# Performance work log

Measured on AMD Instinct MI355X. Metric: run time of the kernel, lower is better.

## Reference

```python
import jax, jax.numpy as jnp
import numpy as np
from jax import lax

K = 5
SCALE = 100.0
IN_CHN = 128
OUT_CHN = 128
KS = 3
STRIDE = 1
PAD = 1
N_W = OUT_CHN * IN_CHN * KS * KS


def setup_inputs() -> dict:
    key = jax.random.key(0)
    k1, k2, k3, k4, k5 = jax.random.split(key, 5)
    x = jax.random.normal(k1, (32, IN_CHN, 56, 56), dtype=jnp.float32)
    Alpha = jax.random.uniform(k2, (OUT_CHN, 1, 1), dtype=jnp.float32)
    # xavier-normal-ish init for M, Z
    M = jax.random.normal(k3, (OUT_CHN, IN_CHN, KS, KS), dtype=jnp.float32) * 0.05
    Z = jax.random.normal(k4, (K, OUT_CHN, IN_CHN, KS, KS), dtype=jnp.float32) * 0.05
    # rv ~ N(0, 1/sqrt(scale)) of shape (1, K); sample is all-zeros so the random branch is taken
    rv = jax.random.normal(k5, (1, K), dtype=jnp.float32) / np.float32(np.sqrt(SCALE))
    return {"x": x, "Alpha": Alpha, "M": M, "Z": Z, "rv": rv}


def reference(x, Alpha, M, Z, rv):
    # --- SDP weight synthesis (normalization is done under no_grad in torch) ---
    m = M.reshape(N_W)                # (N,)
    z = Z.reshape(K, N_W)             # (K, N)
    A = m * m + jnp.sum(z * z, axis=0) / SCALE
    inv = lax.rsqrt(A)
    m_n = m * inv
    z_n = z * inv
    w = (rv @ z_n + m_n).reshape(OUT_CHN, IN_CHN, KS, KS)  # (O,I,k,k)
    # --- sign binarization of weights and activations (ReCU) ---
    bw = jnp.sign(w)
    ba = jnp.sign(x)
    # --- conv2d, NCHW/OIHW ---
    out = lax.conv_general_dilated(
        ba, bw,
        window_strides=(STRIDE, STRIDE),
        padding=[(PAD, PAD), (PAD, PAD)],
        dimension_numbers=("NCHW", "OIHW", "NCHW"),
    )
    out = out * Alpha  # Alpha (O,1,1) broadcasts over (B,O,H,W)
    return out
```

## Files before the change

kernel.cpp:

```cpp
#include <hip/hip_runtime.h>
#include <stdint.h>

typedef unsigned int u32;
typedef unsigned long long u64;

#define NW      147456
#define HW      3136
#define PADW    58
#define PADHW   3364

#define NBI     365
#define NOG     8
#define NBB     440

__global__ __launch_bounds__(256) void k_wsynth(
    const float* __restrict__ M, const float* __restrict__ Z,
    const float* __restrict__ rv, u32* __restrict__ wb)
{
  __shared__ float sw[1152];
  int o = blockIdx.x;
  int t = threadIdx.x;
  float r0 = rv[0], r1 = rv[1], r2 = rv[2], r3 = rv[3], r4 = rv[4];
  const float4* M4 = (const float4*)M;
  const float4* Z4 = (const float4*)Z;
  float4* sw4 = (float4*)sw;

  for (int j = t; j < 288; j += 256) {
    float4 a = M4[o * 288 + j];
    float4 z;
    z = Z4[0 * 36864 + o * 288 + j];
    a.x = fmaf(r0, z.x, a.x); a.y = fmaf(r0, z.y, a.y);
    a.z = fmaf(r0, z.z, a.z); a.w = fmaf(r0, z.w, a.w);
    z = Z4[1 * 36864 + o * 288 + j];
    a.x = fmaf(r1, z.x, a.x); a.y = fmaf(r1, z.y, a.y);
    a.z = fmaf(r1, z.z, a.z); a.w = fmaf(r1, z.w, a.w);
    z = Z4[2 * 36864 + o * 288 + j];
    a.x = fmaf(r2, z.x, a.x); a.y = fmaf(r2, z.y, a.y);
    a.z = fmaf(r2, z.z, a.z); a.w = fmaf(r2, z.w, a.w);
    z = Z4[3 * 36864 + o * 288 + j];
    a.x = fmaf(r3, z.x, a.x); a.y = fmaf(r3, z.y, a.y);
    a.z = fmaf(r3, z.z, a.z); a.w = fmaf(r3, z.w, a.w);
    z = Z4[4 * 36864 + o * 288 + j];
    a.x = fmaf(r4, z.x, a.x); a.y = fmaf(r4, z.y, a.y);
    a.z = fmaf(r4, z.z, a.z); a.w = fmaf(r4, z.w, a.w);
    sw4[j] = a;
  }
  __syncthreads();

  if (t < 36) {
    int tap = t >> 2;
    int wd  = t & 3;
    u32 bits = 0;
#pragma unroll
    for (int c = 0; c < 32; ++c) {
      float v = sw[(wd * 32 + c) * 9 + tap];
      bits |= (v > 0.0f ? 1u : 0u) << c;
    }
    wb[(o * 9 + tap) * 4 + wd] = bits;
  }
}

__global__ __launch_bounds__(256) void k_apack(
    const float* __restrict__ x, u32* __restrict__ abw)
{
  int t     = threadIdx.x;
  int chunk = blockIdx.x % 53;
  int b     = blockIdx.x / 53;
  int px    = chunk * 64 + (t & 63);
  int g     = t >> 6;
  if (px >= PADHW) return;
  int ph = px / PADW;
  int pw = px - ph * PADW;
  u32 bits = 0;
  if (ph >= 1 && ph <= 56 && pw >= 1 && pw <= 56) {
    const float* xp = x + (size_t)b * (128 * HW) + (size_t)g * (32 * HW)
                        + (ph - 1) * 56 + (pw - 1);
#pragma unroll
    for (int c = 0; c < 32; ++c)
      bits |= (xp[(size_t)c * HW] > 0.0f ? 1u : 0u) << c;
  }
  abw[((size_t)b * PADHW + px) * 4 + g] = bits;
}

__global__ __launch_bounds__(256) void k_conv(
    const uint4* __restrict__ ab, const uint4* __restrict__ wbg,
    const float* __restrict__ Alpha, float* __restrict__ out)
{
  int bx  = blockIdx.x;
  int tid = threadIdx.x;

  if (bx < NBI * NOG) {
    int og = bx / NBI;
    int bp = bx - og * NBI;
    int p  = bp * 256 + tid;
    if (p >= 32 * 54 * 54) return;
    int b = p / 2916;
    int r = p - b * 2916;
    int h = 1 + r / 54;
    int w = 1 + (r - (r / 54) * 54);

    const uint4* abp = ab + ((size_t)b * PADW + h) * PADW + w;
    u32 a[9][4];
#pragma unroll
    for (int dh = 0; dh < 3; ++dh)
#pragma unroll
      for (int dw = 0; dw < 3; ++dw) {
        uint4 v = abp[(size_t)dh * PADW + dw];
        int tt = dh * 3 + dw;
        a[tt][0] = v.x; a[tt][1] = v.y; a[tt][2] = v.z; a[tt][3] = v.w;
      }

    float* outp = out + ((size_t)b * 128 + og * 16) * HW + h * 56 + w;
#pragma unroll 2
    for (int oi = 0; oi < 16; ++oi) {
      int o = og * 16 + oi;
      int s = 0;
#pragma unroll
      for (int tt = 0; tt < 9; ++tt) {
        uint4 wv = wbg[o * 9 + tt];
        s += __popc(a[tt][0] ^ wv.x);
        s += __popc(a[tt][1] ^ wv.y);
        s += __popc(a[tt][2] ^ wv.z);
        s += __popc(a[tt][3] ^ wv.w);
      }
      outp[(size_t)oi * HW] = (float)(1152 - 2 * s) * Alpha[o];
    }
  } else {
    int idx = (bx - NBI * NOG) * 256 + tid;
    int og  = idx / 7040;
    int rem = idx - og * 7040;
    int b   = rem / 220;
    int e   = rem - b * 220;
    int h, w;
    if      (e < 56)  { h = 0;  w = e; }
    else if (e < 112) { h = 55; w = e - 56; }
    else if (e < 166) { w = 0;  h = e - 111; }
    else              { w = 55; h = e - 165; }

    u32 a[9][4];
    u32 kk[9];
    int nv = 0;
#pragma unroll
    for (int dh = 0; dh < 3; ++dh)
#pragma unroll
      for (int dw = 0; dw < 3; ++dw) {
        int tt = dh * 3 + dw;
        int hh = h + dh;
        int ww = w + dw;
        uint4 v = ab[((size_t)b * PADW + hh) * PADW + ww];
        a[tt][0] = v.x; a[tt][1] = v.y; a[tt][2] = v.z; a[tt][3] = v.w;
        int valid = (hh >= 1) & (hh <= 56) & (ww >= 1) & (ww <= 56);
        kk[tt] = valid ? 0xffffffffu : 0u;
        nv += valid;
      }
    int base = nv * 128;
    float* outp = out + ((size_t)b * 128 + og * 8) * HW + h * 56 + w;

#pragma unroll 2
    for (int oi = 0; oi < 8; ++oi) {
      int o = og * 8 + oi;
      int s = 0;
#pragma unroll
      for (int tt = 0; tt < 9; ++tt) {
        uint4 wv = wbg[o * 9 + tt];
        s += __popc((a[tt][0] ^ wv.x) & kk[tt]);
        s += __popc((a[tt][1] ^ wv.y) & kk[tt]);
        s += __popc((a[tt][2] ^ wv.z) & kk[tt]);
        s += __popc((a[tt][3] ^ wv.w) & kk[tt]);
      }
      outp[(size_t)oi * HW] = (float)(base - 2 * s) * Alpha[o];
    }
  }
}

extern "C" void kernel_launch(void* const* d_in, const int* in_sizes, int n_in,
                              void* d_out, int out_size, void* d_ws, size_t ws_size,
                              hipStream_t stream)
{
  const float* x     = (const float*)d_in[0];
  const float* Alpha = (const float*)d_in[1];
  const float* M     = (const float*)d_in[2];
  const float* Z     = (const float*)d_in[3];
  const float* rv    = (const float*)d_in[4];
  float* out         = (float*)d_out;

  u32* wb = (u32*)d_ws;
  u32* ab = (u32*)((char*)d_ws + 18432);

  k_wsynth<<<128, 256, 0, stream>>>(M, Z, rv, wb);
  k_apack<<<32 * 53, 256, 0, stream>>>(x, ab);
  k_conv<<<NBI * NOG + NBB, 256, 0, stream>>>((const uint4*)ab, (const uint4*)wb, Alpha, out);
}
```

Baseline: 147.4 us.

## Merge prep kernels, compute four pixels per thread, fold borders into precomputed bias

Weight synthesis and activation packing now run in one launch, so the pipeline has one fewer kernel. The conv kernel gives each thread four adjacent output pixels and reuses a 3x6 window of packed activations across them. Zero-padding edge cases are handled by a per-class bias table (9 border classes) precomputed from weight popcounts, which removes the separate masked border path. Outputs are written as float4. The trade-offs are higher register pressure, about 72 activation words per thread, and fewer threads overall.

New measurement: 136.5 us. 1.08x faster.

```diff
diff --git a/kernel.cpp b/kernel.cpp
--- a/kernel.cpp
+++ b/kernel.cpp
@@ -4,172 +4,178 @@
 typedef unsigned int u32;
 typedef unsigned long long u64;
 
-#define NW      147456
 #define HW      3136
 #define PADW    58
 #define PADHW   3364
 
-#define NBI     365
-#define NOG     8
-#define NBB     440
+#define WB_OFF   0
+#define BF_OFF   18432
+#define N2A_OFF  23040
+#define AB_OFF   23552
 
-__global__ __launch_bounds__(256) void k_wsynth(
+__global__ __launch_bounds__(256) void k_prep(
+    const float* __restrict__ x, const float* __restrict__ Alpha,
     const float* __restrict__ M, const float* __restrict__ Z,
-    const float* __restrict__ rv, u32* __restrict__ wb)
+    const float* __restrict__ rv, char* __restrict__ ws)
 {
-  __shared__ float sw[1152];
-  int o = blockIdx.x;
   int t = threadIdx.x;
-  float r0 = rv[0], r1 = rv[1], r2 = rv[2], r3 = rv[3], r4 = rv[4];
-  const float4* M4 = (const float4*)M;
-  const float4* Z4 = (const float4*)Z;
-  float4* sw4 = (float4*)sw;
+  if (blockIdx.x < 128) {
+    u32*   wb  = (u32*)(ws + WB_OFF);
+    float* Bf  = (float*)(ws + BF_OFF);
+    float* n2a = (float*)(ws + N2A_OFF);
+    __shared__ float sw[1152];
+    __shared__ u32 sbits[36];
+    __shared__ int spc[9];
+    int o = blockIdx.x;
+    float r0 = rv[0], r1 = rv[1], r2 = rv[2], r3 = rv[3], r4 = rv[4];
+    const float4* M4 = (const float4*)M;
+    const float4* Z4 = (const float4*)Z;
+    float4* sw4 = (float4*)sw;
 
-  for (int j = t; j < 288; j += 256) {
-    float4 a = M4[o * 288 + j];
-    float4 z;
-    z = Z4[0 * 36864 + o * 288 + j];
-    a.x = fmaf(r0, z.x, a.x); a.y = fmaf(r0, z.y, a.y);
-    a.z = fmaf(r0, z.z, a.z); a.w = fmaf(r0, z.w, a.w);
-    z = Z4[1 * 36864 + o * 288 + j];
-    a.x = fmaf(r1, z.x, a.x); a.y = fmaf(r1, z.y, a.y);
-    a.z = fmaf(r1, z.z, a.z); a.w = fmaf(r1, z.w, a.w);
-    z = Z4[2 * 36864 + o * 288 + j];
-    a.x = fmaf(r2, z.x, a.x); a.y = fmaf(r2, z.y, a.y);
-    a.z = fmaf(r2, z.z, a.z); a.w = fmaf(r2, z.w, a.w);
-    z = Z4[3 * 36864 + o * 288 + j];
-    a.x = fmaf(r3, z.x, a.x); a.y = fmaf(r3, z.y, a.y);
-    a.z = fmaf(r3, z.z, a.z); a.w = fmaf(r3, z.w, a.w);
-    z = Z4[4 * 36864 + o * 288 + j];
-    a.x = fmaf(r4, z.x, a.x); a.y = fmaf(r4, z.y, a.y);
-    a.z = fmaf(r4, z.z, a.z); a.w = fmaf(r4, z.w, a.w);
-    sw4[j] = a;
+    for (int j = t; j < 288; j += 256) {
+      float4 a = M4[o * 288 + j];
+      float4 z;
+      z = Z4[0 * 36864 + o * 288 + j];
+      a.x = fmaf(r0, z.x, a.x); a.y = fmaf(r0, z.y, a.y);
+      a.z = fmaf(r0, z.z, a.z); a.w = fmaf(r0, z.w, a.w);
+      z = Z4[1 * 36864 + o * 288 + j];
+      a.x = fmaf(r1, z.x, a.x); a.y = fmaf(r1, z.y, a.y);
+      a.z = fmaf(r1, z.z, a.z); a.w = fmaf(r1, z.w, a.w);
+      z = Z4[2 * 36864 + o * 288 + j];
+      a.x = fmaf(r2, z.x, a.x); a.y = fmaf(r2, z.y, a.y);
+      a.z = fmaf(r2, z.z, a.z); a.w = fmaf(r2, z.w, a.w);
+      z = Z4[3 * 36864 + o * 288 + j];
+      a.x = fmaf(r3, z.x, a.x); a.y = fmaf(r3, z.y, a.y);
+      a.z = fmaf(r3, z.z, a.z); a.w = fmaf(r3, z.w, a.w);
+      z = Z4[4 * 36864 + o * 288 + j];
+      a.x = fmaf(r4, z.x, a.x); a.y = fmaf(r4, z.y, a.y);
+      a.z = fmaf(r4, z.z, a.z); a.w = fmaf(r4, z.w, a.w);
+      sw4[j] = a;
+    }
+    __syncthreads();
+
+    if (t < 36) {
+      int tap = t >> 2;
+      int wd  = t & 3;
+      u32 bits = 0;
+#pragma unroll
+      for (int c = 0; c < 32; ++c) {
+        float v = sw[(wd * 32 + c) * 9 + tap];
+        bits |= (v > 0.0f ? 1u : 0u) << c;
+      }
+      wb[(o * 9 + tap) * 4 + wd] = bits;
+      sbits[t] = bits;
+    }
+    __syncthreads();
+    if (t < 9)
+      spc[t] = __popc(sbits[4 * t]) + __popc(sbits[4 * t + 1])
+             + __popc(sbits[4 * t + 2]) + __popc(sbits[4 * t + 3]);
+    __syncthreads();
+    if (t < 9) {
+      int ht = t / 3, wt = t - ht * 3;
+      int corr = 0;
+#pragma unroll
+      for (int tap = 0; tap < 9; ++tap) {
+        int dh = tap / 3, dw = tap - dh * 3;
+        int inv = ((ht == 0) & (dh == 0)) | ((ht == 2) & (dh == 2)) |
+                  ((wt == 0) & (dw == 0)) | ((wt == 2) & (dw == 2));
+        if (inv) corr += 128 - 2 * spc[tap];
+      }
+      Bf[t * 128 + o] = (float)(1152 - corr) * Alpha[o];
+    }
+    if (t == 0) n2a[o] = -2.0f * Alpha[o];
+  } else {
+    u32* abw  = (u32*)(ws + AB_OFF);
+    int bidx  = blockIdx.x - 128;
+    int chunk = bidx % 53;
+    int b     = bidx / 53;
+    int px    = chunk * 64 + (t & 63);
+    int g     = t >> 6;
+    if (px >= PADHW) return;
+    int ph = px / PADW;
+    int pw = px - ph * PADW;
+    u32 bits = 0;
+    if (ph >= 1 && ph <= 56 && pw >= 1 && pw <= 56) {
+      const float* xp = x + (size_t)b * (128 * HW) + (size_t)g * (32 * HW)
+                          + (ph - 1) * 56 + (pw - 1);
+#pragma unroll
+      for (int c = 0; c < 32; ++c)
+        bits |= (xp[(size_t)c * HW] > 0.0f ? 1u : 0u) << c;
+    }
+    abw[((size_t)b * PADHW + px) * 4 + g] = bits;
+  }
+}
+
+__global__ __launch_bounds__(256) void k_conv(
+    const char* __restrict__ ws, float* __restrict__ out)
+{
+  const uint4*  ab  = (const uint4*)(ws + AB_OFF);
+  const uint4*  wbg = (const uint4*)(ws + WB_OFF);
+  const float*  BfG = (const float*)(ws + BF_OFF);
+  const float*  n2a = (const float*)(ws + N2A_OFF);
+
+  __shared__ float sBf[9][8];
+  int tid = threadIdx.x;
+  int bx  = blockIdx.x;
+  int og  = bx / 98;
+  int o0  = og * 8;
+  if (tid < 72) {
+    int cl = tid / 8, oi = tid - cl * 8;
+    sBf[cl][oi] = BfG[cl * 128 + o0 + oi];
   }
   __syncthreads();
 
-  if (t < 36) {
-    int tap = t >> 2;
-    int wd  = t & 3;
-    u32 bits = 0;
+  int q  = (bx - og * 98) * 256 + tid;
+  int b  = q / 784;
+  int r  = q - b * 784;
+  int h  = r / 14;
+  int w4 = r - h * 14;
+  int w0 = w4 * 4;
+
+  const uint4* ap = ab + ((size_t)b * PADW + h) * PADW + w0;
+  u32 A[3][6][4];
 #pragma unroll
-    for (int c = 0; c < 32; ++c) {
-      float v = sw[(wd * 32 + c) * 9 + tap];
-      bits |= (v > 0.0f ? 1u : 0u) << c;
+  for (int rr = 0; rr < 3; ++rr)
+#pragma unroll
+    for (int cc = 0; cc < 6; ++cc) {
+      uint4 v = ap[(size_t)rr * PADW + cc];
+      A[rr][cc][0] = v.x; A[rr][cc][1] = v.y;
+      A[rr][cc][2] = v.z; A[rr][cc][3] = v.w;
     }
-    wb[(o * 9 + tap) * 4 + wd] = bits;
-  }
-}
 
-__global__ __launch_bounds__(256) void k_apack(
-    const float* __restrict__ x, u32* __restrict__ abw)
-{
-  int t     = threadIdx.x;
-  int chunk = blockIdx.x % 53;
-  int b     = blockIdx.x / 53;
-  int px    = chunk * 64 + (t & 63);
-  int g     = t >> 6;
-  if (px >= PADHW) return;
-  int ph = px / PADW;
-  int pw = px - ph * PADW;
-  u32 bits = 0;
-  if (ph >= 1 && ph <= 56 && pw >= 1 && pw <= 56) {
-    const float* xp = x + (size_t)b * (128 * HW) + (size_t)g * (32 * HW)
-                        + (ph - 1) * 56 + (pw - 1);
+  int ht  = (h == 0) ? 0 : (h == 55 ? 6 : 3);
+  int cl0 = ht + ((w0 == 0) ? 0 : 1);
+  int cl1 = ht + 1;
+  int cl3 = ht + ((w0 == 52) ? 2 : 1);
+
+  float* outp = out + ((size_t)b * 128 + o0) * HW + h * 56 + w0;
+
 #pragma unroll
-    for (int c = 0; c < 32; ++c)
-      bits |= (xp[(size_t)c * HW] > 0.0f ? 1u : 0u) << c;
-  }
-  abw[((size_t)b * PADHW + px) * 4 + g] = bits;
-}
-
-__global__ __launch_bounds__(256) void k_conv(
-    const uint4* __restrict__ ab, const uint4* __restrict__ wbg,
-    const float* __restrict__ Alpha, float* __restrict__ out)
-{
-  int bx  = blockIdx.x;
-  int tid = threadIdx.x;
-
-  if (bx < NBI * NOG) {
-    int og = bx / NBI;
-    int bp = bx - og * NBI;
-    int p  = bp * 256 + tid;
-    if (p >= 32 * 54 * 54) return;
-    int b = p / 2916;
-    int r = p - b * 2916;
-    int h = 1 + r / 54;
-    int w = 1 + (r - (r / 54) * 54);
-
-    const uint4* abp = ab + ((size_t)b * PADW + h) * PADW + w;
-    u32 a[9][4];
+  for (int oi = 0; oi < 8; ++oi) {
+    int o = o0 + oi;
+    int s0 = 0, s1 = 0, s2 = 0, s3 = 0;
 #pragma unroll
     for (int dh = 0; dh < 3; ++dh)
 #pragma unroll
       for (int dw = 0; dw < 3; ++dw) {
-        uint4 v = abp[(size_t)dh * PADW + dw];
-        int tt = dh * 3 + dw;
-        a[tt][0] = v.x; a[tt][1] = v.y; a[tt][2] = v.z; a[tt][3] = v.w;
+        uint4 wv = wbg[o * 9 + dh * 3 + dw];
+#pragma unroll
+        for (int k = 0; k < 4; ++k) {
+          u32 wk = (&wv.x)[k];
+          s0 += __popc(A[dh][dw + 0][k] ^ wk);
+          s1 += __popc(A[dh][dw + 1][k] ^ wk);
+          s2 += __popc(A[dh][dw + 2][k] ^ wk);
+          s3 += __popc(A[dh][dw + 3][k] ^ wk);
+        }
       }
-
-    float* outp = out + ((size_t)b * 128 + og * 16) * HW + h * 56 + w;
-#pragma unroll 2
-    for (int oi = 0; oi < 16; ++oi) {
-      int o = og * 16 + oi;
-      int s = 0;
-#pragma unroll
-      for (int tt = 0; tt < 9; ++tt) {
-        uint4 wv = wbg[o * 9 + tt];
-        s += __popc(a[tt][0] ^ wv.x);
-        s += __popc(a[tt][1] ^ wv.y);
-        s += __popc(a[tt][2] ^ wv.z);
-        s += __popc(a[tt][3] ^ wv.w);
-      }
-      outp[(size_t)oi * HW] = (float)(1152 - 2 * s) * Alpha[o];
-    }
-  } else {
-    int idx = (bx - NBI * NOG) * 256 + tid;
-    int og  = idx / 7040;
-    int rem = idx - og * 7040;
-    int b   = rem / 220;
-    int e   = rem - b * 220;
-    int h, w;
-    if      (e < 56)  { h = 0;  w = e; }
-    else if (e < 112) { h = 55; w = e - 56; }
-    else if (e < 166) { w = 0;  h = e - 111; }
-    else              { w = 55; h = e - 165; }
-
-    u32 a[9][4];
-    u32 kk[9];
-    int nv = 0;
-#pragma unroll
-    for (int dh = 0; dh < 3; ++dh)
-#pragma unroll
-      for (int dw = 0; dw < 3; ++dw) {
-        int tt = dh * 3 + dw;
-        int hh = h + dh;
-        int ww = w + dw;
-        uint4 v = ab[((size_t)b * PADW + hh) * PADW + ww];
-        a[tt][0] = v.x; a[tt][1] = v.y; a[tt][2] = v.z; a[tt][3] = v.w;
-        int valid = (hh >= 1) & (hh <= 56) & (ww >= 1) & (ww <= 56);
-        kk[tt] = valid ? 0xffffffffu : 0u;
-        nv += valid;
-      }
-    int base = nv * 128;
-    float* outp = out + ((size_t)b * 128 + og * 8) * HW + h * 56 + w;
-
-#pragma unroll 2
-    for (int oi = 0; oi < 8; ++oi) {
-      int o = og * 8 + oi;
-      int s = 0;
-#pragma unroll
-      for (int tt = 0; tt < 9; ++tt) {
-        uint4 wv = wbg[o * 9 + tt];
-        s += __popc((a[tt][0] ^ wv.x) & kk[tt]);
-        s += __popc((a[tt][1] ^ wv.y) & kk[tt]);
-        s += __popc((a[tt][2] ^ wv.z) & kk[tt]);
-        s += __popc((a[tt][3] ^ wv.w) & kk[tt]);
-      }
-      outp[(size_t)oi * HW] = (float)(base - 2 * s) * Alpha[o];
-    }
+    float na = n2a[o];
+    float4 ov;
+    ov.x = fmaf((float)s0, na, sBf[0][oi] + (sBf[cl0][oi] - sBf[0][oi]));
+    ov.x = fmaf((float)s0, na, sBf[cl0][oi]);
+    ov.y = fmaf((float)s1, na, sBf[cl1][oi]);
+    ov.z = fmaf((float)s2, na, sBf[cl1][oi]);
+    ov.w = fmaf((float)s3, na, sBf[cl3][oi]);
+    *(float4*)(outp + (size_t)oi * HW) = ov;
   }
 }
 
@@ -183,11 +189,8 @@
   const float* Z     = (const float*)d_in[3];
   const float* rv    = (const float*)d_in[4];
   float* out         = (float*)d_out;
+  char*  ws          = (char*)d_ws;
 
-  u32* wb = (u32*)d_ws;
-  u32* ab = (u32*)((char*)d_ws + 18432);
-
-  k_wsynth<<<128, 256, 0, stream>>>(M, Z, rv, wb);
-  k_apack<<<32 * 53, 256, 0, stream>>>(x, ab);
-  k_conv<<<NBI * NOG + NBB, 256, 0, stream>>>((const uint4*)ab, (const uint4*)wb, Alpha, out);
+  k_prep<<<128 + 32 * 53, 256, 0, stream>>>(x, Alpha, M, Z, rv, ws);
+  k_conv<<<16 * 98, 256, 0, stream>>>(ws, out);
 }
```
